# Kernel tuning notes

Hardware: AMD Instinct MI355X
Metric: run time of the kernel (lower is better)

The kernel has to match this reference:

```python
import jax, jax.numpy as jnp
import numpy as np

B, S, D = 8, 2048, 512  # batch, seq_len, lstm_hidden_dim


def setup_inputs() -> dict:
    key = jax.random.key(0)
    kq, kk, kv = jax.random.split(key, 3)
    return {
        "query": jax.random.normal(kq, (B, S, D), dtype=jnp.float32),
        "key": jax.random.normal(kk, (B, S, D), dtype=jnp.float32),
        "value": jax.random.normal(kv, (B, S, D), dtype=jnp.float32),
    }


def reference(query, key, value):
    hidden_dim = query.shape[-1]
    scale = 1.0 / jnp.sqrt(jnp.asarray(hidden_dim, dtype=jnp.float32))
    # scores: [B, S, S]
    scores = jnp.einsum("bqd,bkd->bqk", query, key) * scale
    attention_weights = jax.nn.softmax(scores, axis=-1)
    context = jnp.einsum("bqk,bkd->bqd", attention_weights, value)
    return (context, attention_weights)
```

## Files before the change

### kernel.cpp

```cpp
#include <hip/hip_runtime.h>


constexpr int BATCH = 8;
constexpr int SEQ = 2048;
constexpr int DIM = 512;
constexpr size_t QK_ELEMS = (size_t)BATCH * SEQ * DIM;
constexpr size_t SS_ELEMS = (size_t)BATCH * SEQ * SEQ;

typedef __attribute__((ext_vector_type(8))) short bh8;
typedef __attribute__((ext_vector_type(8))) unsigned short u16x8;
typedef __attribute__((ext_vector_type(4))) float f4acc;

__device__ __forceinline__ short f2bf(float f) {
  union { float f; unsigned u; } v;
  v.f = f;
  unsigned r = (v.u + 0x7FFFu + ((v.u >> 16) & 1u)) >> 16;
  return (short)r;
}

__device__ __forceinline__ float bf2f(unsigned short h) {
  union { unsigned u; float f; } v;
  v.u = (unsigned)h << 16;
  return v.f;
}

__device__ __forceinline__ void glds16(const unsigned short* g,
                                       unsigned short* l) {
  __builtin_amdgcn_global_load_lds(
      (const __attribute__((address_space(1))) unsigned int*)g,
      (__attribute__((address_space(3))) unsigned int*)l, 16, 0, 0);
}

__global__ __launch_bounds__(256) void convert_qk_kernel(
    const float* __restrict__ Q, const float* __restrict__ K,
    unsigned short* __restrict__ Qbf, unsigned short* __restrict__ Kbf) {
  const size_t i = ((size_t)blockIdx.x * 256 + threadIdx.x) * 8;
  const float sc = blockIdx.y ? 1.0f : 0.044194173824159216f;
  const float* src = blockIdx.y ? K : Q;
  unsigned short* dst = blockIdx.y ? Kbf : Qbf;
  float4 a = *(const float4*)(src + i);
  float4 b = *(const float4*)(src + i + 4);
  bh8 o;
  o[0] = f2bf(a.x * sc); o[1] = f2bf(a.y * sc);
  o[2] = f2bf(a.z * sc); o[3] = f2bf(a.w * sc);
  o[4] = f2bf(b.x * sc); o[5] = f2bf(b.y * sc);
  o[6] = f2bf(b.z * sc); o[7] = f2bf(b.w * sc);
  *(bh8*)(dst + i) = o;
}

__global__ __launch_bounds__(256) void transpose_v_kernel(
    const float* __restrict__ V, unsigned short* __restrict__ Vt) {
  __shared__ float tile[32][33];
  const int s0 = blockIdx.x * 32, d0 = blockIdx.y * 32, b = blockIdx.z;
  const float* Vb = V + (size_t)b * SEQ * DIM;
  unsigned short* Vtb = Vt + (size_t)b * DIM * SEQ;
  const int tx = threadIdx.x & 31, ty = threadIdx.x >> 5;
  for (int r = 0; r < 32; r += 8)
    tile[ty + r][tx] = Vb[(size_t)(s0 + ty + r) * DIM + (d0 + tx)];
  __syncthreads();
  for (int r = 0; r < 32; r += 8)
    Vtb[(size_t)(d0 + ty + r) * SEQ + (s0 + tx)] =
        (unsigned short)f2bf(tile[tx][ty + r]);
}

template <int KDIM>
__device__ __forceinline__ void gemm_loop_nt(
    const unsigned short* __restrict__ A, const unsigned short* __restrict__ B,
    unsigned short* sm, f4acc acc[4][4]) {
  const int tid = threadIdx.x, lane = tid & 63, wave = tid >> 6;
  const int wm = (wave & 1) * 64, wn = (wave >> 1) * 64;
  const int srow = wave * 32 + (lane >> 2), scol = (lane & 3) * 8;
  const unsigned short* Ag = A + (size_t)srow * KDIM + scol;
  const unsigned short* Bg = B + (size_t)srow * KDIM + scol;
  unsigned short* As0 = sm;
  unsigned short* As1 = sm + 4096;
  unsigned short* Bs0 = sm + 8192;
  unsigned short* Bs1 = sm + 12288;
  unsigned short* Al0 = As0 + srow * 32 + scol;
  unsigned short* Al1 = As1 + srow * 32 + scol;
  unsigned short* Bl0 = Bs0 + srow * 32 + scol;
  unsigned short* Bl1 = Bs1 + srow * 32 + scol;
  const int fr = lane & 15, fk = (lane >> 4) * 8;
#pragma unroll 2
  for (int k0 = 0; k0 < KDIM; k0 += 64) {
    glds16(Ag + k0,                        Al0);
    glds16(Ag + k0 + (size_t)16 * KDIM,    Al0 + 512);
    glds16(Ag + k0 + 32,                   Al1);
    glds16(Ag + k0 + 32 + (size_t)16 * KDIM, Al1 + 512);
    glds16(Bg + k0,                        Bl0);
    glds16(Bg + k0 + (size_t)16 * KDIM,    Bl0 + 512);
    glds16(Bg + k0 + 32,                   Bl1);
    glds16(Bg + k0 + 32 + (size_t)16 * KDIM, Bl1 + 512);
    __syncthreads();
    bh8 a0[4], a1[4], b0[4], b1[4];
    for (int i = 0; i < 4; ++i) {
      a0[i] = *(const bh8*)(As0 + (wm + i * 16 + fr) * 32 + fk);
      a1[i] = *(const bh8*)(As1 + (wm + i * 16 + fr) * 32 + fk);
      b0[i] = *(const bh8*)(Bs0 + (wn + i * 16 + fr) * 32 + fk);
      b1[i] = *(const bh8*)(Bs1 + (wn + i * 16 + fr) * 32 + fk);
    }
    for (int mi = 0; mi < 4; ++mi)
      for (int ni = 0; ni < 4; ++ni)
        acc[mi][ni] = __builtin_amdgcn_mfma_f32_16x16x32_bf16(
            a0[mi], b0[ni], acc[mi][ni], 0, 0, 0);
    for (int mi = 0; mi < 4; ++mi)
      for (int ni = 0; ni < 4; ++ni)
        acc[mi][ni] = __builtin_amdgcn_mfma_f32_16x16x32_bf16(
            a1[mi], b1[ni], acc[mi][ni], 0, 0, 0);
    __syncthreads();
  }
}

__global__ __launch_bounds__(256) void scores_kernel(
    const unsigned short* __restrict__ Qbf,
    const unsigned short* __restrict__ Kbf,
    unsigned short* __restrict__ Pbf) {
  __shared__ unsigned short sm[16384];
  const int bm = blockIdx.x, bn = blockIdx.y, b = blockIdx.z;
  const int tid = threadIdx.x, lane = tid & 63, wave = tid >> 6;
  const int wm = (wave & 1) * 64, wn = (wave >> 1) * 64;
  f4acc acc[4][4] = {};
  gemm_loop_nt<DIM>(Qbf + ((size_t)b * SEQ + bm * 128) * DIM,
                    Kbf + ((size_t)b * SEQ + bn * 128) * DIM, sm, acc);
  const int cc = lane & 15, rr = (lane >> 4) * 4;
  for (int mi = 0; mi < 4; ++mi)
    for (int ni = 0; ni < 4; ++ni)
      for (int r = 0; r < 4; ++r)
        sm[(wm + mi * 16 + rr + r) * 128 + (wn + ni * 16 + cc)] =
            (unsigned short)f2bf(__expf(acc[mi][ni][r]));
  __syncthreads();
  unsigned short* Pg =
      Pbf + (size_t)b * SEQ * SEQ + (size_t)(bm * 128) * SEQ + bn * 128;
  for (int i = 0; i < 8; ++i) {
    int idx = i * 256 + tid;
    int row = idx >> 4, g = (idx & 15) * 8;
    *(u16x8*)(Pg + (size_t)row * SEQ + g) = *(const u16x8*)(sm + row * 128 + g);
  }
}

__global__ __launch_bounds__(256) void normalize_kernel(
    const unsigned short* __restrict__ Pbf, float* __restrict__ W,
    float* __restrict__ inv_s) {
  const size_t row = blockIdx.x;
  const int tid = threadIdx.x, lane = tid & 63, wave = tid >> 6;
  u16x8 v = *(const u16x8*)(Pbf + row * SEQ + tid * 8);
  float x[8];
  float s = 0.f;
  for (int j = 0; j < 8; ++j) { x[j] = bf2f(v[j]); s += x[j]; }
  for (int off = 32; off > 0; off >>= 1) s += __shfl_xor(s, off);
  __shared__ float reds[4];
  if (lane == 0) reds[wave] = s;
  __syncthreads();
  s = reds[0] + reds[1] + reds[2] + reds[3];
  const float inv = 1.0f / s;
  if (tid == 0) inv_s[row] = inv;
  float4 o0 = {x[0] * inv, x[1] * inv, x[2] * inv, x[3] * inv};
  float4 o1 = {x[4] * inv, x[5] * inv, x[6] * inv, x[7] * inv};
  float* Wr = W + row * SEQ + tid * 8;
  *(float4*)Wr = o0;
  *(float4*)(Wr + 4) = o1;
}

__global__ __launch_bounds__(256) void context_kernel(
    const unsigned short* __restrict__ Pbf,
    const unsigned short* __restrict__ Vt,
    const float* __restrict__ inv_s, float* __restrict__ C) {
  __shared__ unsigned short sm[16384];
  const int bm = blockIdx.x, bn = blockIdx.y, b = blockIdx.z;
  const int tid = threadIdx.x, lane = tid & 63, wave = tid >> 6;
  const int wm = (wave & 1) * 64, wn = (wave >> 1) * 64;
  f4acc acc[4][4] = {};
  gemm_loop_nt<SEQ>(Pbf + ((size_t)b * SEQ + bm * 128) * SEQ,
                    Vt + ((size_t)b * DIM + bn * 128) * SEQ, sm, acc);
  float* Cb = C + (size_t)b * SEQ * DIM + (size_t)(bm * 128) * DIM + bn * 128;
  const float* invb = inv_s + (size_t)b * SEQ + bm * 128;
  const int cc = lane & 15, rr = (lane >> 4) * 4;
  for (int mi = 0; mi < 4; ++mi) {
    float iv[4];
    for (int r = 0; r < 4; ++r) iv[r] = invb[wm + mi * 16 + rr + r];
    for (int ni = 0; ni < 4; ++ni)
      for (int r = 0; r < 4; ++r)
        Cb[(size_t)(wm + mi * 16 + rr + r) * DIM + (wn + ni * 16 + cc)] =
            acc[mi][ni][r] * iv[r];
  }
}

extern "C" void kernel_launch(void* const* d_in, const int* in_sizes, int n_in,
                              void* d_out, int out_size, void* d_ws,
                              size_t ws_size, hipStream_t stream) {
  const float* Q = (const float*)d_in[0];
  const float* K = (const float*)d_in[1];
  const float* V = (const float*)d_in[2];
  float* C = (float*)d_out;
  float* W = (float*)d_out + QK_ELEMS;
  unsigned short* Qbf = (unsigned short*)d_ws;
  unsigned short* Kbf = Qbf + QK_ELEMS;
  unsigned short* Vt  = Kbf + QK_ELEMS;
  unsigned short* Pbf = Vt + QK_ELEMS;
  float* inv_s = (float*)(Pbf + SS_ELEMS);

  convert_qk_kernel<<<dim3((unsigned)(QK_ELEMS / 8 / 256), 2), 256, 0, stream>>>(
      Q, K, Qbf, Kbf);
  transpose_v_kernel<<<dim3(SEQ / 32, DIM / 32, BATCH), 256, 0, stream>>>(V, Vt);
  scores_kernel<<<dim3(SEQ / 128, SEQ / 128, BATCH), 256, 0, stream>>>(Qbf, Kbf, Pbf);
  normalize_kernel<<<dim3(BATCH * SEQ), 256, 0, stream>>>(Pbf, W, inv_s);
  context_kernel<<<dim3(SEQ / 128, DIM / 128, BATCH), 256, 0, stream>>>(Pbf, Vt, inv_s, C);
}
```

Before: 349.7 us.

## Replace scores GEMM with 256x256-tile, 8-wave pipelined kernel with swizzled LDS

The QK^T scores kernel becomes a 512-thread kernel that computes 256x256 tiles. It uses a multi-stage global-to-LDS prefetch pipeline with explicit vmcnt waits and barriers, XOR-swizzled LDS layouts to avoid bank conflicts, s_setprio around the MFMA bursts, and a block-id swizzle for locality. The aim is to raise data reuse and overlap loads with MFMA in the scores GEMM, which was a major cost. In exchange it uses 128KB of LDS per block, keeps more accumulator registers live, and relies on hand-written waitcnt logic that is fragile.

```diff
diff --git a/kernel.cpp b/kernel.cpp
--- a/kernel.cpp
+++ b/kernel.cpp
@@ -61,6 +61,110 @@
   for (int r = 0; r < 32; r += 8)
     Vtb[(size_t)(d0 + ty + r) * SEQ + (s0 + tx)] =
         (unsigned short)f2bf(tile[tx][ty + r]);
+}
+
+__global__ __launch_bounds__(512, 2) void scores8_kernel(
+    const unsigned short* __restrict__ Qbf,
+    const unsigned short* __restrict__ Kbf,
+    unsigned short* __restrict__ Pbf) {
+  __shared__ __align__(16) unsigned short sm[65536];
+  const int id = blockIdx.x;
+  const int swz = (id & 7) * 64 + (id >> 3);
+  const int b = swz >> 6, local = swz & 63, bm = local & 7, bn = local >> 3;
+  const int tid = threadIdx.x, lane = tid & 63, wave = tid >> 6;
+  const int wm = (wave >> 2) * 128, wn = (wave & 3) * 64;
+  const int fr = lane & 15, c16 = lane >> 4;
+  const int r0 = tid >> 2;
+  const int cbs = (((tid & 3) ^ (r0 & 3)) << 3);
+  const unsigned short* Ag =
+      Qbf + ((size_t)b * SEQ + bm * 256 + r0) * DIM + cbs;
+  const unsigned short* Bg =
+      Kbf + ((size_t)b * SEQ + bn * 256 + r0) * DIM + cbs;
+  unsigned short* smt = sm + tid * 8;
+
+  auto stage = [&](int h) {
+    const int T = h >> 2, part = h & 3;
+    const unsigned short* src =
+        ((part & 1) ? Bg : Ag) + T * 64 + (part >> 1) * 32;
+    unsigned short* l = smt + (T & 1) * 32768 + (part & 1) * 16384 +
+                        ((part >> 1) ^ ((part & 1) ? 0 : 0)) * 8192;
+    l = smt + (T & 1) * 32768 + (part & 1) * 16384 + (part >> 1) * 8192;
+    glds16(src, l);
+    glds16(src + (size_t)128 * DIM, l + 4096);
+  };
+
+  f4acc acc[8][4] = {};
+
+#define PHASE(SLOT, SLICE, MIB, STAGE_STMT, GATE_STMT)                        \
+  {                                                                           \
+    bh8 a[4], bfr[4];                                                         \
+    const unsigned short* As = sm + (SLOT)*32768 + (SLICE)*8192;              \
+    const unsigned short* Bs = As + 16384;                                    \
+    _Pragma("unroll") for (int i = 0; i < 4; ++i) {                           \
+      const int ra = wm + ((MIB) + i) * 16 + fr;                              \
+      a[i] = *(const bh8*)(As + ra * 32 + ((c16 ^ (ra & 3)) << 3));           \
+      const int rb = wn + i * 16 + fr;                                        \
+      bfr[i] = *(const bh8*)(Bs + rb * 32 + ((c16 ^ (rb & 3)) << 3));         \
+    }                                                                         \
+    STAGE_STMT;                                                               \
+    asm volatile("s_barrier" ::: "memory");                                   \
+    asm volatile("s_waitcnt lgkmcnt(0)" ::: "memory");                        \
+    __builtin_amdgcn_s_setprio(1);                                            \
+    _Pragma("unroll") for (int mi = 0; mi < 4; ++mi)                          \
+      _Pragma("unroll") for (int ni = 0; ni < 4; ++ni)                        \
+        acc[(MIB) + mi][ni] = __builtin_amdgcn_mfma_f32_16x16x32_bf16(        \
+            a[mi], bfr[ni], acc[(MIB) + mi][ni], 0, 0, 0);                    \
+    __builtin_amdgcn_s_setprio(0);                                            \
+    GATE_STMT;                                                                \
+    asm volatile("s_barrier" ::: "memory");                                   \
+  }
+
+  stage(0); stage(1); stage(2); stage(3);
+  asm volatile("s_waitcnt vmcnt(4)" ::: "memory");
+  stage(4); stage(5); stage(6);
+  asm volatile("s_waitcnt vmcnt(6)" ::: "memory");
+  asm volatile("s_barrier" ::: "memory");
+
+  int hs = 7;
+#pragma unroll 1
+  for (int it = 0; it < 4; ++it) {
+    PHASE(0, 0, 0, if (hs < 32) stage(hs++), )
+    PHASE(0, 0, 4, if (hs < 32) stage(hs++), )
+    PHASE(0, 1, 0, if (hs < 32) stage(hs++), )
+    PHASE(0, 1, 4, if (hs < 32) stage(hs++),
+          if (it == 3) { asm volatile("s_waitcnt vmcnt(0)" ::: "memory"); }
+          else { asm volatile("s_waitcnt vmcnt(6)" ::: "memory"); })
+    PHASE(1, 0, 0, if (hs < 32) stage(hs++), )
+    PHASE(1, 0, 4, if (hs < 32) stage(hs++), )
+    PHASE(1, 1, 0, if (hs < 32) stage(hs++), )
+    PHASE(1, 1, 4, if (hs < 32) stage(hs++),
+          if (it < 3) { asm volatile("s_waitcnt vmcnt(6)" ::: "memory"); })
+  }
+#undef PHASE
+
+  __syncthreads();
+  const int rl = (lane >> 4) << 2, cl = lane & 15;
+#pragma unroll
+  for (int mi = 0; mi < 8; ++mi)
+#pragma unroll
+    for (int ni = 0; ni < 4; ++ni)
+#pragma unroll
+      for (int r = 0; r < 4; ++r) {
+        const int row = wm + mi * 16 + rl + r;
+        const int col = wn + ni * 16 + cl;
+        sm[row * 256 + (((col >> 3) ^ (row & 7)) << 3) + (col & 7)] =
+            (unsigned short)f2bf(__expf(acc[mi][ni][r]));
+      }
+  __syncthreads();
+  unsigned short* Pg =
+      Pbf + (size_t)b * SEQ * SEQ + (size_t)(bm * 256) * SEQ + bn * 256;
+#pragma unroll
+  for (int i = 0; i < 16; ++i) {
+    const int idx = i * 512 + tid;
+    const int row = idx >> 5, ch = idx & 31;
+    *(u16x8*)(Pg + (size_t)row * SEQ + ch * 8) =
+        *(const u16x8*)(sm + row * 256 + ((ch ^ (row & 7)) << 3));
+  }
 }
 
 template <int KDIM>
@@ -111,33 +215,6 @@
   }
 }
 
-__global__ __launch_bounds__(256) void scores_kernel(
-    const unsigned short* __restrict__ Qbf,
-    const unsigned short* __restrict__ Kbf,
-    unsigned short* __restrict__ Pbf) {
-  __shared__ unsigned short sm[16384];
-  const int bm = blockIdx.x, bn = blockIdx.y, b = blockIdx.z;
-  const int tid = threadIdx.x, lane = tid & 63, wave = tid >> 6;
-  const int wm = (wave & 1) * 64, wn = (wave >> 1) * 64;
-  f4acc acc[4][4] = {};
-  gemm_loop_nt<DIM>(Qbf + ((size_t)b * SEQ + bm * 128) * DIM,
-                    Kbf + ((size_t)b * SEQ + bn * 128) * DIM, sm, acc);
-  const int cc = lane & 15, rr = (lane >> 4) * 4;
-  for (int mi = 0; mi < 4; ++mi)
-    for (int ni = 0; ni < 4; ++ni)
-      for (int r = 0; r < 4; ++r)
-        sm[(wm + mi * 16 + rr + r) * 128 + (wn + ni * 16 + cc)] =
-            (unsigned short)f2bf(__expf(acc[mi][ni][r]));
-  __syncthreads();
-  unsigned short* Pg =
-      Pbf + (size_t)b * SEQ * SEQ + (size_t)(bm * 128) * SEQ + bn * 128;
-  for (int i = 0; i < 8; ++i) {
-    int idx = i * 256 + tid;
-    int row = idx >> 4, g = (idx & 15) * 8;
-    *(u16x8*)(Pg + (size_t)row * SEQ + g) = *(const u16x8*)(sm + row * 128 + g);
-  }
-}
-
 __global__ __launch_bounds__(256) void normalize_kernel(
     const unsigned short* __restrict__ Pbf, float* __restrict__ W,
     float* __restrict__ inv_s) {
@@ -202,7 +279,7 @@
   convert_qk_kernel<<<dim3((unsigned)(QK_ELEMS / 8 / 256), 2), 256, 0, stream>>>(
       Q, K, Qbf, Kbf);
   transpose_v_kernel<<<dim3(SEQ / 32, DIM / 32, BATCH), 256, 0, stream>>>(V, Vt);
-  scores_kernel<<<dim3(SEQ / 128, SEQ / 128, BATCH), 256, 0, stream>>>(Qbf, Kbf, Pbf);
+  scores8_kernel<<<dim3(512), 512, 0, stream>>>(Qbf, Kbf, Pbf);
   normalize_kernel<<<dim3(BATCH * SEQ), 256, 0, stream>>>(Pbf, W, inv_s);
   context_kernel<<<dim3(SEQ / 128, DIM / 128, BATCH), 256, 0, stream>>>(Pbf, Vt, inv_s, C);
 }
```

Measured after the change: 357.2 us. 2.2% more time.

## Rewrite context GEMM with 256x128 tiles, triple-buffered LDS pipeline and XCD remap

Applied to the files above, without the earlier changes.

The context kernel now runs 512-thread blocks, each computing a 256x128 output tile. LDS is triple-buffered so global-to-LDS loads for step k+2 are issued while MFMAs consume step k, with explicit vmcnt waits and barriers instead of full syncthreads around each load. Block IDs are remapped so each group of consecutive IDs shares a batch. The goals are to hide memory latency, raise reuse per block, and improve L2 locality. The cost is 144KB of LDS per block and 256 blocks in total, which may leave some CUs underused.

```diff
diff --git a/kernel.cpp b/kernel.cpp
--- a/kernel.cpp
+++ b/kernel.cpp
@@ -161,24 +161,88 @@
   *(float4*)(Wr + 4) = o1;
 }
 
-__global__ __launch_bounds__(256) void context_kernel(
+__global__ __launch_bounds__(512, 2) void context_kernel(
     const unsigned short* __restrict__ Pbf,
     const unsigned short* __restrict__ Vt,
     const float* __restrict__ inv_s, float* __restrict__ C) {
-  __shared__ unsigned short sm[16384];
-  const int bm = blockIdx.x, bn = blockIdx.y, b = blockIdx.z;
-  const int tid = threadIdx.x, lane = tid & 63, wave = tid >> 6;
-  const int wm = (wave & 1) * 64, wn = (wave >> 1) * 64;
+  __shared__ __align__(16) unsigned short sm[73728];
+  const int id = blockIdx.x;
+  const int logical = (id & 7) * 32 + (id >> 3);
+  const int b = logical >> 5, bm = (logical >> 2) & 7, bn = logical & 3;
+  const int tid = threadIdx.x, lane = tid & 63, wave = tid >> 6;
+  const int wm = (wave >> 1) * 64, wn = (wave & 1) * 64;
+  const unsigned short* A = Pbf + ((size_t)b * SEQ + bm * 256) * SEQ;
+  const unsigned short* Bv = Vt + ((size_t)b * DIM + bn * 128) * SEQ;
+  const int srow = tid >> 2, scol = (tid & 3) * 8;
+  const unsigned short* Ag = A + (size_t)srow * SEQ + scol;
+  const unsigned short* Bg = Bv + (size_t)srow * SEQ + scol;
+  unsigned short* smt = sm + tid * 8;
+
+  auto stageS = [&](int q, int s, int kt) {
+    const unsigned short* ga = Ag + kt * 64 + s * 32;
+    unsigned short* la = smt + q * 24576 + s * 8192;
+    glds16(ga, la);
+    glds16(ga + (size_t)128 * SEQ, la + 4096);
+    glds16(Bg + kt * 64 + s * 32, smt + q * 24576 + 16384 + s * 4096);
+  };
+
   f4acc acc[4][4] = {};
-  gemm_loop_nt<SEQ>(Pbf + ((size_t)b * SEQ + bm * 128) * SEQ,
-                    Vt + ((size_t)b * DIM + bn * 128) * SEQ, sm, acc);
-  float* Cb = C + (size_t)b * SEQ * DIM + (size_t)(bm * 128) * DIM + bn * 128;
-  const float* invb = inv_s + (size_t)b * SEQ + bm * 128;
+  const int fr = lane & 15, fk = (lane >> 4) * 8;
+
+  stageS(0, 0, 0); stageS(0, 1, 0);
+  stageS(1, 0, 1); stageS(1, 1, 1);
+  asm volatile("s_waitcnt vmcnt(6)" ::: "memory");
+  __builtin_amdgcn_s_barrier();
+
+  int q0 = 0, q2 = 2;
+#pragma unroll 1
+  for (int kt = 0; kt < 32; ++kt) {
+    const unsigned short* buf = sm + q0 * 24576;
+#pragma unroll
+    for (int s = 0; s < 2; ++s) {
+      bh8 a[4], bb[4];
+      const unsigned short* As = buf + s * 8192;
+      const unsigned short* Bs = buf + 16384 + s * 4096;
+#pragma unroll
+      for (int i = 0; i < 4; ++i) {
+        a[i]  = *(const bh8*)(As + (wm + i * 16 + fr) * 32 + fk);
+        bb[i] = *(const bh8*)(Bs + (wn + i * 16 + fr) * 32 + fk);
+      }
+      if (kt < 30) stageS(q2, s, kt + 2);
+      __builtin_amdgcn_s_barrier();
+      asm volatile("s_waitcnt lgkmcnt(0)" ::: "memory");
+      __builtin_amdgcn_sched_barrier(0);
+      __builtin_amdgcn_s_setprio(1);
+#pragma unroll
+      for (int mi = 0; mi < 4; ++mi)
+#pragma unroll
+        for (int ni = 0; ni < 4; ++ni)
+          acc[mi][ni] = __builtin_amdgcn_mfma_f32_16x16x32_bf16(
+              a[mi], bb[ni], acc[mi][ni], 0, 0, 0);
+      __builtin_amdgcn_s_setprio(0);
+      if (s == 1) {
+        if (kt < 30) {
+          asm volatile("s_waitcnt vmcnt(6)" ::: "memory");
+        } else if (kt == 30) {
+          asm volatile("s_waitcnt vmcnt(0)" ::: "memory");
+        }
+      }
+      __builtin_amdgcn_s_barrier();
+    }
+    q0 = (q0 == 2) ? 0 : q0 + 1;
+    q2 = (q2 == 2) ? 0 : q2 + 1;
+  }
+
+  float* Cb = C + (size_t)b * SEQ * DIM + (size_t)(bm * 256) * DIM + bn * 128;
+  const float* invb = inv_s + (size_t)b * SEQ + bm * 256;
   const int cc = lane & 15, rr = (lane >> 4) * 4;
+#pragma unroll
   for (int mi = 0; mi < 4; ++mi) {
     float iv[4];
     for (int r = 0; r < 4; ++r) iv[r] = invb[wm + mi * 16 + rr + r];
+#pragma unroll
     for (int ni = 0; ni < 4; ++ni)
+#pragma unroll
       for (int r = 0; r < 4; ++r)
         Cb[(size_t)(wm + mi * 16 + rr + r) * DIM + (wn + ni * 16 + cc)] =
             acc[mi][ni][r] * iv[r];
@@ -204,5 +268,5 @@
   transpose_v_kernel<<<dim3(SEQ / 32, DIM / 32, BATCH), 256, 0, stream>>>(V, Vt);
   scores_kernel<<<dim3(SEQ / 128, SEQ / 128, BATCH), 256, 0, stream>>>(Qbf, Kbf, Pbf);
   normalize_kernel<<<dim3(BATCH * SEQ), 256, 0, stream>>>(Pbf, W, inv_s);
-  context_kernel<<<dim3(SEQ / 128, DIM / 128, BATCH), 256, 0, stream>>>(Pbf, Vt, inv_s, C);
-}
+  context_kernel<<<dim3(256), 512, 0, stream>>>(Pbf, Vt, inv_s, C);
+}
```

Measured after the change: 348.3 us. About the same (-0.4%).
